# Optimization experiments

Hardware: AMD Instinct MI355X
Metric: run time of the kernel (lower is better)

## Reference

```python
import jax, jax.numpy as jnp
import numpy as np

B, PS, D, HEADS, HD, PROP = 16, 32, 768, 8, 24, 4
N = PS * PS          # 1024 tokens
M = PROP * PROP      # 16 proposal centers
INNER = HEADS * HD   # 192
HID = 4 * D          # 3072
EPS = 1e-12


def setup_inputs() -> dict:
    key = jax.random.key(0)
    ks = jax.random.split(key, 8)
    s = 0.02
    f32 = jnp.float32
    return {
        "x": jax.random.normal(ks[0], (B, N, D), f32),
        "ln1_w": jnp.ones((D,), f32), "ln1_b": jnp.zeros((D,), f32),
        "f_w": jax.random.normal(ks[1], (INNER, D), f32) * s, "f_b": jnp.zeros((INNER,), f32),
        "v_w": jax.random.normal(ks[2], (INNER, D), f32) * s, "v_b": jnp.zeros((INNER,), f32),
        "proj_w": jax.random.normal(ks[3], (D, INNER), f32) * s, "proj_b": jnp.zeros((D,), f32),
        "sim_alpha": jnp.ones((1,), f32), "sim_beta": jnp.zeros((1,), f32),
        "ln2_w": jnp.ones((D,), f32), "ln2_b": jnp.zeros((D,), f32),
        "fc1_w": jax.random.normal(ks[4], (HID, D), f32) * s, "fc1_b": jnp.zeros((HID,), f32),
        "fc2_w": jax.random.normal(ks[5], (D, HID), f32) * s, "fc2_b": jnp.zeros((D,), f32),
    }


def _ln(x, w, b):
    mu = x.mean(-1, keepdims=True)
    var = ((x - mu) ** 2).mean(-1, keepdims=True)
    return (x - mu) / jnp.sqrt(var + 1e-5) * w + b


def _cluster2d(x, f_w, f_b, v_w, v_b, proj_w, proj_b, alpha, beta):
    b = x.shape[0]
    xi = x.reshape(b, PS, PS, D).transpose(0, 3, 1, 2)  # b c w h
    # 1x1 convs f and v
    f = jnp.einsum('oc,bcwh->bowh', f_w, xi) + f_b[None, :, None, None]
    v = jnp.einsum('oc,bcwh->bowh', v_w, xi) + v_b[None, :, None, None]
    # split heads: (b e) c w h
    f = f.reshape(b * HEADS, HD, PS, PS)
    v = v.reshape(b * HEADS, HD, PS, PS)
    # adaptive avg pool to (PROP, PROP) -- exact kernel/stride pooling since PS % PROP == 0
    s = PS // PROP
    cen = f.reshape(-1, HD, PROP, s, PROP, s).mean((3, 5))  # be c 4 4
    vcen = v.reshape(-1, HD, PROP, s, PROP, s).mean((3, 5)).reshape(-1, HD, M).transpose(0, 2, 1)  # be M c
    cf = cen.reshape(-1, HD, M).transpose(0, 2, 1)  # be M c
    xf = f.reshape(-1, HD, N).transpose(0, 2, 1)    # be N c
    # pairwise euclidean similarity on L2-normalized vectors: ||a-b|| = sqrt(2 - 2 a.b)
    cn = cf / jnp.maximum(jnp.linalg.norm(cf, axis=-1, keepdims=True), EPS)
    xn = xf / jnp.maximum(jnp.linalg.norm(xf, axis=-1, keepdims=True), EPS)
    dist = jnp.sqrt(jnp.clip(2.0 - 2.0 * jnp.einsum('bmc,bnc->bmn', cn, xn), EPS, None))
    sim = jax.nn.leaky_relu(beta + alpha * jnp.exp(-dist), 0.2)  # be M N (dropout eval = identity)
    # top-1 hard assignment (torch scatter of argmax -> one-hot mask, no grad through mask)
    mask = jax.nn.one_hot(jnp.argmax(sim, axis=1), M, dtype=sim.dtype).transpose(0, 2, 1)  # be M N
    sim = sim * mask
    v2 = v.reshape(-1, HD, N).transpose(0, 2, 1)  # be N c
    # weighted reduce to centers, then broadcast back to tokens
    outc = (jnp.einsum('bmn,bnc->bmc', sim, v2) + vcen) / (mask.sum(-1, keepdims=True) + 1.0)  # be M c
    out = jnp.einsum('bmn,bmc->bnc', sim, outc)  # be N c
    out = out.reshape(-1, PS, PS, HD).transpose(0, 3, 1, 2).reshape(b, INNER, PS, PS)
    out = jnp.einsum('oc,bcwh->bowh', proj_w, out) + proj_b[None, :, None, None]
    return out.transpose(0, 2, 3, 1).reshape(b, N, D)


def reference(x, ln1_w, ln1_b, f_w, f_b, v_w, v_b, proj_w, proj_b, sim_alpha, sim_beta,
              ln2_w, ln2_b, fc1_w, fc1_b, fc2_w, fc2_b):
    h = x + _cluster2d(_ln(x, ln1_w, ln1_b), f_w, f_b, v_w, v_b, proj_w, proj_b, sim_alpha, sim_beta)
    y = _ln(h, ln2_w, ln2_b)
    y = jax.nn.gelu(jnp.einsum('bnd,hd->bnh', y, fc1_w) + fc1_b, approximate=False)
    y = jnp.einsum('bnh,dh->bnd', y, fc2_w) + fc2_b
    return h + y
```

## Files before the change

### kernel.cpp

```cpp
#include <hip/hip_runtime.h>
#include <hip/hip_bf16.h>
#include <cmath>

typedef unsigned short u16;
typedef short short8 __attribute__((ext_vector_type(8)));
typedef float f32x4 __attribute__((ext_vector_type(4)));

#define D_ 768
#define NTOK 16384
#define INNER_ 192
#define HID_ 3072

__device__ __forceinline__ float u2f(u16 u) { return __uint_as_float((unsigned)u << 16); }
__device__ __forceinline__ u16 f2u(float f) {
  __hip_bfloat16 h = __float2bfloat16(f);
  u16 u; __builtin_memcpy(&u, &h, 2); return u;
}
__device__ __forceinline__ float ld1(const void* p, size_t i, int f32) {
  return f32 ? ((const float*)p)[i] : u2f(((const u16*)p)[i]);
}
__device__ __forceinline__ void st1(void* p, size_t i, float v, int f32) {
  if (f32) ((float*)p)[i] = v; else ((u16*)p)[i] = f2u(v);
}
__device__ __forceinline__ float gelu_exact(float v) {
  return 0.5f * v * (1.f + erff(v * 0.7071067811865476f));
}
__device__ __forceinline__ void unpack8(const uint4 v, float* o) {
  o[0] = u2f((u16)(v.x & 0xffffu)); o[1] = u2f((u16)(v.x >> 16));
  o[2] = u2f((u16)(v.y & 0xffffu)); o[3] = u2f((u16)(v.y >> 16));
  o[4] = u2f((u16)(v.z & 0xffffu)); o[5] = u2f((u16)(v.z >> 16));
  o[6] = u2f((u16)(v.w & 0xffffu)); o[7] = u2f((u16)(v.w >> 16));
}

__global__ __launch_bounds__(64) void detect_kernel(const unsigned* __restrict__ x,
                                                    int* __restrict__ flag) {
  int cnt = 0;
  for (int i = threadIdx.x; i < 512; i += 64) {
    const unsigned e0 = (x[i] >> 7) & 0xFFu;
    if (e0 >= 96u && e0 <= 144u) cnt++;
  }
#pragma unroll
  for (int o = 32; o > 0; o >>= 1) cnt += __shfl_down(cnt, o);
  if (threadIdx.x == 0) flag[0] = (cnt < 256) ? 1 : 0;
}

struct CvtJob { const void* src; u16* dst; int n4; };
struct CvtArgs { CvtJob j[10]; };

__global__ __launch_bounds__(256) void cvt_kernel(CvtArgs a, const int* __restrict__ flagp) {
  const int f32 = flagp[0];
  const CvtJob jb = a.j[blockIdx.y];
  const int i = blockIdx.x * 256 + threadIdx.x;
  if (i >= jb.n4) return;
  if (f32) {
    const float4 v = ((const float4*)jb.src)[i];
    const unsigned lo = (unsigned)f2u(v.x) | ((unsigned)f2u(v.y) << 16);
    const unsigned hi = (unsigned)f2u(v.z) | ((unsigned)f2u(v.w) << 16);
    ((uint2*)jb.dst)[i] = make_uint2(lo, hi);
  } else {
    ((uint2*)jb.dst)[i] = ((const uint2*)jb.src)[i];
  }
}

__global__ __launch_bounds__(256) void ln_kernel(const void* __restrict__ x,
                                                 const void* __restrict__ w,
                                                 const void* __restrict__ b,
                                                 u16* __restrict__ y,
                                                 const int* __restrict__ flagp) {
  const int fl = flagp[0];
  const size_t t = blockIdx.x;
  float v[3];
  float s = 0.f, s2 = 0.f;
#pragma unroll
  for (int i = 0; i < 3; i++) {
    v[i] = ld1(x, t * D_ + threadIdx.x + 256 * i, fl);
    s += v[i];
    s2 += v[i] * v[i];
  }
#pragma unroll
  for (int o = 32; o > 0; o >>= 1) {
    s += __shfl_down(s, o);
    s2 += __shfl_down(s2, o);
  }
  __shared__ float ps[4], ps2[4];
  __shared__ float smu, srstd;
  const int wid = threadIdx.x >> 6, lane = threadIdx.x & 63;
  if (lane == 0) { ps[wid] = s; ps2[wid] = s2; }
  __syncthreads();
  if (threadIdx.x == 0) {
    const float a = ps[0] + ps[1] + ps[2] + ps[3];
    const float a2 = ps2[0] + ps2[1] + ps2[2] + ps2[3];
    const float mu = a * (1.f / D_);
    smu = mu;
    srstd = rsqrtf(a2 * (1.f / D_) - mu * mu + 1e-5f);
  }
  __syncthreads();
  const float mu = smu, rstd = srstd;
#pragma unroll
  for (int i = 0; i < 3; i++) {
    const int c = threadIdx.x + 256 * i;
    y[t * D_ + c] = f2u((v[i] - mu) * rstd * ld1(w, c, fl) + ld1(b, c, fl));
  }
}

template <int EPI>
__global__ __launch_bounds__(256) void mfma_gemm(const u16* __restrict__ A, int lda,
                                                 const u16* __restrict__ B, int ldb,
                                                 const u16* __restrict__ bias,
                                                 const void* __restrict__ res,
                                                 void* __restrict__ C, int ldc,
                                                 int K, int row0,
                                                 const int* __restrict__ flagp) {
  const int fl = flagp[0];
  __shared__ __align__(16) u16 Asb[128 * 32];
  __shared__ __align__(16) u16 Bsb[128 * 32];
  const int tid = threadIdx.x;
  const int lane = tid & 63;
  const int wv = tid >> 6;
  const int bm = blockIdx.x * 128;
  const int bn = blockIdx.y * 128;
  const int wm = (wv & 1) * 64;
  const int wn = (wv >> 1) * 64;
  const int c0 = tid, c1 = tid + 256;
  const u16* Ag0 = A + (size_t)(bm + (c0 >> 2)) * lda + (c0 & 3) * 8;
  const u16* Ag1 = A + (size_t)(bm + (c1 >> 2)) * lda + (c1 & 3) * 8;
  const u16* Bg0 = B + (size_t)(bn + (c0 >> 2)) * ldb + (c0 & 3) * 8;
  const u16* Bg1 = B + (size_t)(bn + (c1 >> 2)) * ldb + (c1 & 3) * 8;
  u16* la0 = &Asb[c0 * 8];
  u16* la1 = &Asb[c1 * 8];
  u16* lb0 = &Bsb[c0 * 8];
  u16* lb1 = &Bsb[c1 * 8];

  f32x4 acc[4][4];
#pragma unroll
  for (int i = 0; i < 4; i++)
#pragma unroll
    for (int j = 0; j < 4; j++) acc[i][j] = (f32x4){0.f, 0.f, 0.f, 0.f};

  const int ml = lane & 15;
  const int kq = (lane >> 4) * 8;

  for (int k0 = 0; k0 < K; k0 += 32) {
    __syncthreads();
    __builtin_amdgcn_global_load_lds(
        (const __attribute__((address_space(1))) void*)(Ag0 + k0),
        (__attribute__((address_space(3))) void*)la0, 16, 0, 0);
    __builtin_amdgcn_global_load_lds(
        (const __attribute__((address_space(1))) void*)(Ag1 + k0),
        (__attribute__((address_space(3))) void*)la1, 16, 0, 0);
    __builtin_amdgcn_global_load_lds(
        (const __attribute__((address_space(1))) void*)(Bg0 + k0),
        (__attribute__((address_space(3))) void*)lb0, 16, 0, 0);
    __builtin_amdgcn_global_load_lds(
        (const __attribute__((address_space(1))) void*)(Bg1 + k0),
        (__attribute__((address_space(3))) void*)lb1, 16, 0, 0);
    __syncthreads();
    short8 af[4], bf[4];
#pragma unroll
    for (int i = 0; i < 4; i++) {
      af[i] = *(const short8*)&Asb[(wm + i * 16 + ml) * 32 + kq];
      bf[i] = *(const short8*)&Bsb[(wn + i * 16 + ml) * 32 + kq];
    }
#pragma unroll
    for (int i = 0; i < 4; i++)
#pragma unroll
      for (int j = 0; j < 4; j++)
        acc[i][j] = __builtin_amdgcn_mfma_f32_16x16x32_bf16(af[i], bf[j], acc[i][j], 0, 0, 0);
  }

  const int qr = (lane >> 4) * 4;
#pragma unroll
  for (int i = 0; i < 4; i++) {
#pragma unroll
    for (int j = 0; j < 4; j++) {
      const int colg = bn + wn + j * 16 + ml;
      const float bb = u2f(bias[colg]);
#pragma unroll
      for (int r = 0; r < 4; r++) {
        const size_t row = (size_t)row0 + bm + wm + i * 16 + qr + r;
        float v = acc[i][j][r] + bb;
        if (EPI == 1) v = gelu_exact(v);
        if (EPI == 2) {
          v += ld1(res, row * ldc + colg, fl);
          st1(C, row * ldc + colg, v, fl);
        } else {
          ((u16*)C)[row * ldc + colg] = f2u(v);
        }
      }
    }
  }
}

#define SB8 __builtin_amdgcn_sched_barrier(0)
#define BAR8 __builtin_amdgcn_s_barrier()

template <int EPI>
__global__ __launch_bounds__(512, 4) void mfma_gemmP(const u16* __restrict__ A, int lda,
                                                     const u16* __restrict__ B, int ldb,
                                                     const u16* __restrict__ bias,
                                                     const void* __restrict__ res,
                                                     void* __restrict__ C, int ldc,
                                                     int K, int row0, int gm, int gn,
                                                     const int* __restrict__ flagp) {
  const int fl = flagp[0];
  __shared__ __align__(16) u16 L[3][(128 + 256) * 32];
  const int tid = threadIdx.x;
  const int lane = tid & 63;
  const int wv = tid >> 6;

  int mb_, nb_;
  {
    const int bid = blockIdx.x;
    const int ntot = gm * gn;
    if ((ntot & 511) == 0 && (512 % gm) == 0 && gm >= 2) {
      const int l = bid >> 8, p = bid & 255;
      const int G = gm >> 1;
      nb_ = (l >> 1) * (512 / gm) + p / G;
      mb_ = (p % G) * 2 + (l & 1);
    } else {
      mb_ = bid % gm;
      nb_ = bid / gm;
    }
  }
  const int bm = mb_ * 128;
  const int bn = nb_ * 256;

  const int wm = (wv & 1) * 64;
  const int wn = (wv >> 1) * 64;
  const int ml = lane & 15;
  const int qk = lane >> 4;

  const int srow = tid >> 2;
  const int q_s = (tid & 3) ^ ((srow >> 1) & 3);
  const size_t gaA  = (size_t)(bm + srow) * lda + q_s * 8;
  const size_t gbB0 = (size_t)(bn + srow) * ldb + q_s * 8;
  const size_t gbB1 = (size_t)(bn + srow + 128) * ldb + q_s * 8;

  int offA[4], offB[4];
#pragma unroll
  for (int i = 0; i < 4; i++) {
    const int r = wm + i * 16 + ml;
    offA[i] = (r * 4 + (qk ^ ((r >> 1) & 3))) * 8;
  }
#pragma unroll
  for (int j = 0; j < 4; j++) {
    const int r = wn + j * 16 + ml;
    offB[j] = 4096 + (r * 4 + (qk ^ ((r >> 1) & 3))) * 8;
  }

  f32x4 acc[4][4];
#pragma unroll
  for (int i = 0; i < 4; i++)
#pragma unroll
    for (int j = 0; j < 4; j++) acc[i][j] = (f32x4){0.f, 0.f, 0.f, 0.f};

  const int NT = K >> 5;

#define STGP(tilex) do {                                                            \
    const size_t k_ = (size_t)(tilex) * 32;                                         \
    u16* lb_ = &L[(tilex) % 3][0];                                                  \
    __builtin_amdgcn_global_load_lds(                                               \
        (const __attribute__((address_space(1))) void*)(A + gaA + k_),              \
        (__attribute__((address_space(3))) void*)(lb_ + tid * 8), 16, 0, 0);        \
    __builtin_amdgcn_global_load_lds(                                               \
        (const __attribute__((address_space(1))) void*)(B + gbB0 + k_),             \
        (__attribute__((address_space(3))) void*)(lb_ + 4096 + tid * 8), 16, 0, 0); \
    __builtin_amdgcn_global_load_lds(                                               \
        (const __attribute__((address_space(1))) void*)(B + gbB1 + k_),             \
        (__attribute__((address_space(3))) void*)(lb_ + 4096 + (tid + 512) * 8), 16, 0, 0); \
  } while (0)

  STGP(0);
  if (NT > 1) {
    STGP(1);
    asm volatile("s_waitcnt vmcnt(3)" ::: "memory");
  } else {
    asm volatile("s_waitcnt vmcnt(0)" ::: "memory");
  }
  SB8; BAR8; SB8;

  for (int t = 0; t < NT; t++) {
    const u16* Lb = &L[t % 3][0];
    short8 af[4], bf[4];
#pragma unroll
    for (int j = 0; j < 4; j++) bf[j] = *(const short8*)(Lb + offB[j]);
#pragma unroll
    for (int i = 0; i < 4; i++) af[i] = *(const short8*)(Lb + offA[i]);
    if (t + 2 < NT) {
      STGP(t + 2);
      asm volatile("s_waitcnt vmcnt(3)" ::: "memory");
    } else if (t + 1 < NT) {
      asm volatile("s_waitcnt vmcnt(0)" ::: "memory");
    }
    SB8; BAR8;
    asm volatile("s_waitcnt lgkmcnt(0)" ::: "memory"); SB8;
    __builtin_amdgcn_s_setprio(1);
#pragma unroll
    for (int i = 0; i < 4; i++)
#pragma unroll
      for (int j = 0; j < 4; j++)
        acc[i][j] = __builtin_amdgcn_mfma_f32_16x16x32_bf16(af[i], bf[j], acc[i][j], 0, 0, 0);
    __builtin_amdgcn_s_setprio(0);
    SB8; BAR8;
  }
#undef STGP

  const int qr = (lane >> 4) * 4;
#pragma unroll
  for (int i = 0; i < 4; i++) {
#pragma unroll
    for (int j = 0; j < 4; j++) {
      const int colg = bn + wn + j * 16 + ml;
      const float bb = u2f(bias[colg]);
#pragma unroll
      for (int r = 0; r < 4; r++) {
        const size_t row = (size_t)row0 + bm + wm + i * 16 + qr + r;
        float v = acc[i][j][r] + bb;
        if (EPI == 1) v = gelu_exact(v);
        if (EPI == 2) {
          v += ld1(res, row * ldc + colg, fl);
          st1(C, row * ldc + colg, v, fl);
        } else {
          ((u16*)C)[row * ldc + colg] = f2u(v);
        }
      }
    }
  }
}

__global__ __launch_bounds__(512) void cluster_kernel(u16* __restrict__ FV,
                                                      const void* __restrict__ alpha_p,
                                                      const void* __restrict__ beta_p,
                                                      const int* __restrict__ flagp) {
  const int fl = flagp[0];
  const int be = blockIdx.x;
  const int b = be >> 3, e = be & 7;
  const int tid = threadIdx.x;
  const float alpha = ld1(alpha_p, 0, fl), beta = ld1(beta_p, 0, fl);

  __shared__ __align__(16) u16 S[1024 * 24];
  __shared__ float cn[16][24];
  __shared__ float vcen[16][24];
  __shared__ float outc[16][24];
  __shared__ float rcn[16];
  __shared__ int cnt[16];

  u16* Fg = FV + ((size_t)b * 1024) * 384 + e * 24;
  const u16* Vg = Fg + 192;

  for (int c = tid; c < 3072; c += 512) {
    const int n = c / 3, q = c - n * 3;
    *(uint4*)&S[n * 24 + q * 8] = *(const uint4*)(Fg + (size_t)n * 384 + q * 8);
  }
  if (tid < 16) cnt[tid] = 0;
  __syncthreads();

  for (int t = tid; t < 384; t += 512) {
    const int m = t / 24, ch = t - m * 24;
    const int pw = m >> 2, ph = m & 3;
    float sum = 0.f;
    for (int dw = 0; dw < 8; dw++) {
      const int base = (pw * 8 + dw) * 32 + ph * 8;
      for (int dh = 0; dh < 8; dh++) sum += u2f(S[(base + dh) * 24 + ch]);
    }
    cn[m][ch] = sum * (1.f / 64.f);
  }
  __syncthreads();
  if (tid < 16) {
    float s = 0.f;
    for (int ch = 0; ch < 24; ch++) { const float v = cn[tid][ch]; s += v * v; }
    rcn[tid] = 1.f / fmaxf(sqrtf(s), 1e-12f);
  }
  __syncthreads();

  const int na = tid, nb = tid + 512;
  float besta = -3.4e38f, bestb = -3.4e38f;
  int bma = 0, bmb = 0;
  {
    float xa[24], xb[24];
    const uint4* ra = (const uint4*)&S[na * 24];
    const uint4* rb = (const uint4*)&S[nb * 24];
#pragma unroll
    for (int q = 0; q < 3; q++) {
      unpack8(ra[q], &xa[q * 8]);
      unpack8(rb[q], &xb[q * 8]);
    }
    float ssa = 0.f, ssb = 0.f;
#pragma unroll
    for (int ch = 0; ch < 24; ch++) {
      ssa = fmaf(xa[ch], xa[ch], ssa);
      ssb = fmaf(xb[ch], xb[ch], ssb);
    }
    const float rna = 1.f / fmaxf(sqrtf(ssa), 1e-12f);
    const float rnb = 1.f / fmaxf(sqrtf(ssb), 1e-12f);
    for (int m = 0; m < 16; m++) {
      float da = 0.f, db = 0.f;
#pragma unroll
      for (int k = 0; k < 12; k++) {
        const float2 c = *(const float2*)&cn[m][2 * k];
        da = fmaf(c.x, xa[2 * k], da); da = fmaf(c.y, xa[2 * k + 1], da);
        db = fmaf(c.x, xb[2 * k], db); db = fmaf(c.y, xb[2 * k + 1], db);
      }
      const float rc = rcn[m];
      da *= rna * rc;
      db *= rnb * rc;
      const float dda = sqrtf(fmaxf(2.f - 2.f * da, 1e-12f));
      const float ddb = sqrtf(fmaxf(2.f - 2.f * db, 1e-12f));
      const float za = beta + alpha * expf(-dda);
      const float zb = beta + alpha * expf(-ddb);
      const float sa = (za >= 0.f) ? za : 0.2f * za;
      const float sb = (zb >= 0.f) ? zb : 0.2f * zb;
      if (sa > besta) { besta = sa; bma = m; }
      if (sb > bestb) { bestb = sb; bmb = m; }
    }
    atomicAdd(&cnt[bma], 1);
    atomicAdd(&cnt[bmb], 1);
  }
  __syncthreads();

  for (int c = tid; c < 3072; c += 512) {
    const int n = c / 3, q = c - n * 3;
    *(uint4*)&S[n * 24 + q * 8] = *(const uint4*)(Vg + (size_t)n * 384 + q * 8);
  }
  if (tid < 384) outc[tid / 24][tid - (tid / 24) * 24] = 0.f;
  __syncthreads();

  for (int t = tid; t < 384; t += 512) {
    const int m = t / 24, ch = t - m * 24;
    const int pw = m >> 2, ph = m & 3;
    float sum = 0.f;
    for (int dw = 0; dw < 8; dw++) {
      const int base = (pw * 8 + dw) * 32 + ph * 8;
      for (int dh = 0; dh < 8; dh++) sum += u2f(S[(base + dh) * 24 + ch]);
    }
    vcen[m][ch] = sum * (1.f / 64.f);
  }

  {
    float va[24], vb[24];
    const uint4* ra = (const uint4*)&S[na * 24];
    const uint4* rb = (const uint4*)&S[nb * 24];
#pragma unroll
    for (int q = 0; q < 3; q++) {
      unpack8(ra[q], &va[q * 8]);
      unpack8(rb[q], &vb[q * 8]);
    }
#pragma unroll
    for (int ch = 0; ch < 24; ch++) {
      atomicAdd(&outc[bma][ch], besta * va[ch]);
      atomicAdd(&outc[bmb][ch], bestb * vb[ch]);
    }
  }
  __syncthreads();

  for (int t = tid; t < 384; t += 512) {
    const int m = t / 24, ch = t - m * 24;
    outc[m][ch] = (outc[m][ch] + vcen[m][ch]) / ((float)cnt[m] + 1.f);
  }
  __syncthreads();

#pragma unroll
  for (int pass = 0; pass < 2; pass++) {
    const int n = pass ? nb : na;
    const int m = pass ? bmb : bma;
    const float s = pass ? bestb : besta;
    unsigned w[12];
#pragma unroll
    for (int k = 0; k < 12; k++) {
      w[k] = (unsigned)f2u(s * outc[m][2 * k]) |
             ((unsigned)f2u(s * outc[m][2 * k + 1]) << 16);
    }
    uint4* dst = (uint4*)(Fg + (size_t)n * 384);
    dst[0] = make_uint4(w[0], w[1], w[2], w[3]);
    dst[1] = make_uint4(w[4], w[5], w[6], w[7]);
    dst[2] = make_uint4(w[8], w[9], w[10], w[11]);
  }
}

extern "C" void kernel_launch(void* const* d_in, const int* in_sizes, int n_in,
                              void* d_out, int out_size, void* d_ws, size_t ws_size,
                              hipStream_t stream) {
  const void* x      = d_in[0];
  const void* ln1_w  = d_in[1];
  const void* ln1_b  = d_in[2];
  const void* f_w    = d_in[3];
  const void* f_b    = d_in[4];
  const void* v_w    = d_in[5];
  const void* v_b    = d_in[6];
  const void* proj_w = d_in[7];
  const void* proj_b = d_in[8];
  const void* alpha  = d_in[9];
  const void* beta   = d_in[10];
  const void* ln2_w  = d_in[11];
  const void* ln2_b  = d_in[12];
  const void* fc1_w  = d_in[13];
  const void* fc1_b  = d_in[14];
  const void* fc2_w  = d_in[15];
  const void* fc2_b  = d_in[16];

  char* ws = (char*)d_ws;
  int* flag  = (int*)(ws + 0);
  u16* fvw   = (u16*)(ws + 256);
  u16* prw   = (u16*)(ws + 590080);
  u16* f1w   = (u16*)(ws + 884992);
  u16* f2w   = (u16*)(ws + 5603584);
  u16* fvb   = (u16*)(ws + 10322176);
  u16* prb   = (u16*)(ws + 10322944);
  u16* f1b   = (u16*)(ws + 10324480);
  u16* f2b_  = (u16*)(ws + 10330624);
  u16* Y1    = (u16*)(ws + 10332416);
  u16* FV    = (u16*)(ws + 35498240);
  u16* Gext  = (u16*)(ws + 48081152);

  const long extra = (long)ws_size - 48081152L;
  u16* G; long crows;
  if (extra >= (long)NTOK * HID_ * 2) { G = Gext; crows = NTOK; }
  else if (extra >= 256L * HID_ * 2) { G = Gext; crows = (extra / (HID_ * 2)) / 256 * 256; }
  else { G = FV; crows = 2048; }

  detect_kernel<<<1, 64, 0, stream>>>((const unsigned*)x, flag);

  CvtArgs ca;
  ca.j[0] = {f_w,    fvw,            147456 / 4};
  ca.j[1] = {v_w,    fvw + 147456,   147456 / 4};
  ca.j[2] = {proj_w, prw,            147456 / 4};
  ca.j[3] = {fc1_w,  f1w,            2359296 / 4};
  ca.j[4] = {fc2_w,  f2w,            2359296 / 4};
  ca.j[5] = {f_b,    fvb,            192 / 4};
  ca.j[6] = {v_b,    fvb + 192,      192 / 4};
  ca.j[7] = {proj_b, prb,            768 / 4};
  ca.j[8] = {fc1_b,  f1b,            3072 / 4};
  ca.j[9] = {fc2_b,  f2b_,           768 / 4};
  cvt_kernel<<<dim3(2304, 10), 256, 0, stream>>>(ca, flag);

  ln_kernel<<<NTOK, 256, 0, stream>>>(x, ln1_w, ln1_b, Y1, flag);
  mfma_gemm<0><<<dim3(128, 3), 256, 0, stream>>>(
      Y1, D_, fvw, D_, fvb, nullptr, FV, 384, D_, 0, flag);
  cluster_kernel<<<128, 512, 0, stream>>>(FV, alpha, beta, flag);
  mfma_gemm<2><<<dim3(128, 6), 256, 0, stream>>>(
      FV, 384, prw, INNER_, prb, x, d_out, D_, INNER_, 0, flag);
  ln_kernel<<<NTOK, 256, 0, stream>>>(d_out, ln2_w, ln2_b, Y1, flag);
  for (long t0 = 0; t0 < NTOK; t0 += crows) {
    const long ct = (t0 + crows <= NTOK) ? crows : (NTOK - t0);
    const int gm1 = (int)(ct / 128), gn1 = HID_ / 256;
    const int gm2 = (int)(ct / 128), gn2 = D_ / 256;
    mfma_gemmP<1><<<dim3(gm1 * gn1), 512, 0, stream>>>(
        Y1 + t0 * D_, D_, f1w, D_, f1b, nullptr, G, HID_, D_, 0, gm1, gn1, flag);
    mfma_gemmP<2><<<dim3(gm2 * gn2), 512, 0, stream>>>(
        G, HID_, f2w, HID_, f2b_, d_out, d_out, D_, HID_, (int)t0, gm2, gn2, flag);
  }
}
```

Baseline: 488.1 us.

## Retile MLP GEMMs to 256x128 blocks and restructure cluster kernel

Replaces the 512-thread 128x256 MLP GEMM, which used a swizzled block order, with a 256-thread 256x128 tile kernel. Each wave now holds an 8x4 MFMA accumulator grid, which raises per-wave register pressure and drops the block remapping meant for L2 locality. The cluster kernel now runs 1024 threads, one token each, and loads F and V into separate LDS buffers so the two centroid pools are computed in one pass. It writes results to a new CL buffer instead of overwriting FV, which changes the projection GEMM's A stride and shifts the workspace layout.

New measurement: 530.7 us. +8.7%, slower.

```diff
diff --git a/kernel.cpp b/kernel.cpp
--- a/kernel.cpp
+++ b/kernel.cpp
@@ -195,85 +195,82 @@
 #define BAR8 __builtin_amdgcn_s_barrier()
 
 template <int EPI>
-__global__ __launch_bounds__(512, 4) void mfma_gemmP(const u16* __restrict__ A, int lda,
+__global__ __launch_bounds__(256, 2) void mfma_gemmQ(const u16* __restrict__ A, int lda,
                                                      const u16* __restrict__ B, int ldb,
                                                      const u16* __restrict__ bias,
                                                      const void* __restrict__ res,
                                                      void* __restrict__ C, int ldc,
-                                                     int K, int row0, int gm, int gn,
+                                                     int K, int row0,
                                                      const int* __restrict__ flagp) {
   const int fl = flagp[0];
-  __shared__ __align__(16) u16 L[3][(128 + 256) * 32];
+  __shared__ __align__(16) u16 L[3][(256 + 128) * 32];
   const int tid = threadIdx.x;
   const int lane = tid & 63;
   const int wv = tid >> 6;
 
-  int mb_, nb_;
-  {
-    const int bid = blockIdx.x;
-    const int ntot = gm * gn;
-    if ((ntot & 511) == 0 && (512 % gm) == 0 && gm >= 2) {
-      const int l = bid >> 8, p = bid & 255;
-      const int G = gm >> 1;
-      nb_ = (l >> 1) * (512 / gm) + p / G;
-      mb_ = (p % G) * 2 + (l & 1);
-    } else {
-      mb_ = bid % gm;
-      nb_ = bid / gm;
-    }
-  }
-  const int bm = mb_ * 128;
-  const int bn = nb_ * 256;
-
-  const int wm = (wv & 1) * 64;
+  const int bm = blockIdx.x * 256;
+  const int bn = blockIdx.y * 128;
+
+  const int wm = (wv & 1) * 128;
   const int wn = (wv >> 1) * 64;
   const int ml = lane & 15;
   const int qk = lane >> 4;
 
   const int srow = tid >> 2;
   const int q_s = (tid & 3) ^ ((srow >> 1) & 3);
-  const size_t gaA  = (size_t)(bm + srow) * lda + q_s * 8;
-  const size_t gbB0 = (size_t)(bn + srow) * ldb + q_s * 8;
-  const size_t gbB1 = (size_t)(bn + srow + 128) * ldb + q_s * 8;
-
-  int offA[4], offB[4];
-#pragma unroll
-  for (int i = 0; i < 4; i++) {
+  size_t gA[4], gB[2];
+#pragma unroll
+  for (int p = 0; p < 4; p++) gA[p] = (size_t)(bm + srow + 64 * p) * lda + q_s * 8;
+#pragma unroll
+  for (int p = 0; p < 2; p++) gB[p] = (size_t)(bn + srow + 64 * p) * ldb + q_s * 8;
+
+  int offA[8], offB[4];
+#pragma unroll
+  for (int i = 0; i < 8; i++) {
     const int r = wm + i * 16 + ml;
     offA[i] = (r * 4 + (qk ^ ((r >> 1) & 3))) * 8;
   }
 #pragma unroll
   for (int j = 0; j < 4; j++) {
     const int r = wn + j * 16 + ml;
-    offB[j] = 4096 + (r * 4 + (qk ^ ((r >> 1) & 3))) * 8;
-  }
-
-  f32x4 acc[4][4];
-#pragma unroll
-  for (int i = 0; i < 4; i++)
+    offB[j] = 8192 + (r * 4 + (qk ^ ((r >> 1) & 3))) * 8;
+  }
+
+  f32x4 acc[8][4];
+#pragma unroll
+  for (int i = 0; i < 8; i++)
 #pragma unroll
     for (int j = 0; j < 4; j++) acc[i][j] = (f32x4){0.f, 0.f, 0.f, 0.f};
 
   const int NT = K >> 5;
 
-#define STGP(tilex) do {                                                            \
+#define STGQ(tilex) do {                                                            \
     const size_t k_ = (size_t)(tilex) * 32;                                         \
     u16* lb_ = &L[(tilex) % 3][0];                                                  \
     __builtin_amdgcn_global_load_lds(                                               \
-        (const __attribute__((address_space(1))) void*)(A + gaA + k_),              \
+        (const __attribute__((address_space(1))) void*)(A + gA[0] + k_),            \
         (__attribute__((address_space(3))) void*)(lb_ + tid * 8), 16, 0, 0);        \
     __builtin_amdgcn_global_load_lds(                                               \
-        (const __attribute__((address_space(1))) void*)(B + gbB0 + k_),             \
-        (__attribute__((address_space(3))) void*)(lb_ + 4096 + tid * 8), 16, 0, 0); \
+        (const __attribute__((address_space(1))) void*)(A + gA[1] + k_),            \
+        (__attribute__((address_space(3))) void*)(lb_ + (tid + 256) * 8), 16, 0, 0);\
     __builtin_amdgcn_global_load_lds(                                               \
-        (const __attribute__((address_space(1))) void*)(B + gbB1 + k_),             \
-        (__attribute__((address_space(3))) void*)(lb_ + 4096 + (tid + 512) * 8), 16, 0, 0); \
+        (const __attribute__((address_space(1))) void*)(A + gA[2] + k_),            \
+        (__attribute__((address_space(3))) void*)(lb_ + (tid + 512) * 8), 16, 0, 0);\
+    __builtin_amdgcn_global_load_lds(                                               \
+        (const __attribute__((address_space(1))) void*)(A + gA[3] + k_),            \
+        (__attribute__((address_space(3))) void*)(lb_ + (tid + 768) * 8), 16, 0, 0);\
+    __builtin_amdgcn_global_load_lds(                                               \
+        (const __attribute__((address_space(1))) void*)(B + gB[0] + k_),            \
+        (__attribute__((address_space(3))) void*)(lb_ + 8192 + tid * 8), 16, 0, 0); \
+    __builtin_amdgcn_global_load_lds(                                               \
+        (const __attribute__((address_space(1))) void*)(B + gB[1] + k_),            \
+        (__attribute__((address_space(3))) void*)(lb_ + 8192 + (tid + 256) * 8), 16, 0, 0); \
   } while (0)
 
-  STGP(0);
+  STGQ(0);
   if (NT > 1) {
-    STGP(1);
-    asm volatile("s_waitcnt vmcnt(3)" ::: "memory");
+    STGQ(1);
+    asm volatile("s_waitcnt vmcnt(6)" ::: "memory");
   } else {
     asm volatile("s_waitcnt vmcnt(0)" ::: "memory");
   }
@@ -281,14 +278,14 @@
 
   for (int t = 0; t < NT; t++) {
     const u16* Lb = &L[t % 3][0];
-    short8 af[4], bf[4];
+    short8 af[8], bf[4];
 #pragma unroll
     for (int j = 0; j < 4; j++) bf[j] = *(const short8*)(Lb + offB[j]);
 #pragma unroll
-    for (int i = 0; i < 4; i++) af[i] = *(const short8*)(Lb + offA[i]);
+    for (int i = 0; i < 8; i++) af[i] = *(const short8*)(Lb + offA[i]);
     if (t + 2 < NT) {
-      STGP(t + 2);
-      asm volatile("s_waitcnt vmcnt(3)" ::: "memory");
+      STGQ(t + 2);
+      asm volatile("s_waitcnt vmcnt(6)" ::: "memory");
     } else if (t + 1 < NT) {
       asm volatile("s_waitcnt vmcnt(0)" ::: "memory");
     }
@@ -296,18 +293,18 @@
     asm volatile("s_waitcnt lgkmcnt(0)" ::: "memory"); SB8;
     __builtin_amdgcn_s_setprio(1);
 #pragma unroll
-    for (int i = 0; i < 4; i++)
+    for (int i = 0; i < 8; i++)
 #pragma unroll
       for (int j = 0; j < 4; j++)
         acc[i][j] = __builtin_amdgcn_mfma_f32_16x16x32_bf16(af[i], bf[j], acc[i][j], 0, 0, 0);
     __builtin_amdgcn_s_setprio(0);
     SB8; BAR8;
   }
-#undef STGP
+#undef STGQ
 
   const int qr = (lane >> 4) * 4;
 #pragma unroll
-  for (int i = 0; i < 4; i++) {
+  for (int i = 0; i < 8; i++) {
 #pragma unroll
     for (int j = 0; j < 4; j++) {
       const int colg = bn + wn + j * 16 + ml;
@@ -328,42 +325,50 @@
   }
 }
 
-__global__ __launch_bounds__(512) void cluster_kernel(u16* __restrict__ FV,
-                                                      const void* __restrict__ alpha_p,
-                                                      const void* __restrict__ beta_p,
-                                                      const int* __restrict__ flagp) {
+__global__ __launch_bounds__(1024) void cluster_kernel(const u16* __restrict__ FV,
+                                                       u16* __restrict__ CL,
+                                                       const void* __restrict__ alpha_p,
+                                                       const void* __restrict__ beta_p,
+                                                       const int* __restrict__ flagp) {
   const int fl = flagp[0];
   const int be = blockIdx.x;
   const int b = be >> 3, e = be & 7;
   const int tid = threadIdx.x;
   const float alpha = ld1(alpha_p, 0, fl), beta = ld1(beta_p, 0, fl);
 
-  __shared__ __align__(16) u16 S[1024 * 24];
+  __shared__ __align__(16) u16 SF[1024 * 24];
+  __shared__ __align__(16) u16 SV[1024 * 24];
   __shared__ float cn[16][24];
   __shared__ float vcen[16][24];
   __shared__ float outc[16][24];
   __shared__ float rcn[16];
   __shared__ int cnt[16];
 
-  u16* Fg = FV + ((size_t)b * 1024) * 384 + e * 24;
+  const u16* Fg = FV + ((size_t)b * 1024) * 384 + e * 24;
   const u16* Vg = Fg + 192;
-
-  for (int c = tid; c < 3072; c += 512) {
+  u16* Cg = CL + ((size_t)b * 1024) * 192 + e * 24;
+
+  for (int c = tid; c < 3072; c += 1024) {
     const int n = c / 3, q = c - n * 3;
-    *(uint4*)&S[n * 24 + q * 8] = *(const uint4*)(Fg + (size_t)n * 384 + q * 8);
+    *(uint4*)&SF[n * 24 + q * 8] = *(const uint4*)(Fg + (size_t)n * 384 + q * 8);
+    *(uint4*)&SV[n * 24 + q * 8] = *(const uint4*)(Vg + (size_t)n * 384 + q * 8);
   }
   if (tid < 16) cnt[tid] = 0;
-  __syncthreads();
-
-  for (int t = tid; t < 384; t += 512) {
+  if (tid < 384) outc[tid / 24][tid - (tid / 24) * 24] = 0.f;
+  __syncthreads();
+
+  if (tid < 768) {
+    const int t = tid & 383;
     const int m = t / 24, ch = t - m * 24;
     const int pw = m >> 2, ph = m & 3;
+    const u16* src = (tid < 384) ? SF : SV;
     float sum = 0.f;
     for (int dw = 0; dw < 8; dw++) {
       const int base = (pw * 8 + dw) * 32 + ph * 8;
-      for (int dh = 0; dh < 8; dh++) sum += u2f(S[(base + dh) * 24 + ch]);
-    }
-    cn[m][ch] = sum * (1.f / 64.f);
+      for (int dh = 0; dh < 8; dh++) sum += u2f(src[(base + dh) * 24 + ch]);
+    }
+    if (tid < 384) cn[m][ch] = sum * (1.f / 64.f);
+    else           vcen[m][ch] = sum * (1.f / 64.f);
   }
   __syncthreads();
   if (tid < 16) {
@@ -373,104 +378,55 @@
   }
   __syncthreads();
 
-  const int na = tid, nb = tid + 512;
-  float besta = -3.4e38f, bestb = -3.4e38f;
-  int bma = 0, bmb = 0;
+  const int n = tid;
+  float best = -3.4e38f;
+  int bm_ = 0;
   {
-    float xa[24], xb[24];
-    const uint4* ra = (const uint4*)&S[na * 24];
-    const uint4* rb = (const uint4*)&S[nb * 24];
-#pragma unroll
-    for (int q = 0; q < 3; q++) {
-      unpack8(ra[q], &xa[q * 8]);
-      unpack8(rb[q], &xb[q * 8]);
-    }
-    float ssa = 0.f, ssb = 0.f;
-#pragma unroll
-    for (int ch = 0; ch < 24; ch++) {
-      ssa = fmaf(xa[ch], xa[ch], ssa);
-      ssb = fmaf(xb[ch], xb[ch], ssb);
-    }
-    const float rna = 1.f / fmaxf(sqrtf(ssa), 1e-12f);
-    const float rnb = 1.f / fmaxf(sqrtf(ssb), 1e-12f);
+    float xf[24];
+    const uint4* ra = (const uint4*)&SF[n * 24];
+#pragma unroll
+    for (int q = 0; q < 3; q++) unpack8(ra[q], &xf[q * 8]);
+    float ss = 0.f;
+#pragma unroll
+    for (int ch = 0; ch < 24; ch++) ss = fmaf(xf[ch], xf[ch], ss);
+    const float rn = 1.f / fmaxf(sqrtf(ss), 1e-12f);
     for (int m = 0; m < 16; m++) {
-      float da = 0.f, db = 0.f;
+      float d = 0.f;
 #pragma unroll
       for (int k = 0; k < 12; k++) {
         const float2 c = *(const float2*)&cn[m][2 * k];
-        da = fmaf(c.x, xa[2 * k], da); da = fmaf(c.y, xa[2 * k + 1], da);
-        db = fmaf(c.x, xb[2 * k], db); db = fmaf(c.y, xb[2 * k + 1], db);
+        d = fmaf(c.x, xf[2 * k], d); d = fmaf(c.y, xf[2 * k + 1], d);
       }
-      const float rc = rcn[m];
-      da *= rna * rc;
-      db *= rnb * rc;
-      const float dda = sqrtf(fmaxf(2.f - 2.f * da, 1e-12f));
-      const float ddb = sqrtf(fmaxf(2.f - 2.f * db, 1e-12f));
-      const float za = beta + alpha * expf(-dda);
-      const float zb = beta + alpha * expf(-ddb);
-      const float sa = (za >= 0.f) ? za : 0.2f * za;
-      const float sb = (zb >= 0.f) ? zb : 0.2f * zb;
-      if (sa > besta) { besta = sa; bma = m; }
-      if (sb > bestb) { bestb = sb; bmb = m; }
-    }
-    atomicAdd(&cnt[bma], 1);
-    atomicAdd(&cnt[bmb], 1);
-  }
-  __syncthreads();
-
-  for (int c = tid; c < 3072; c += 512) {
-    const int n = c / 3, q = c - n * 3;
-    *(uint4*)&S[n * 24 + q * 8] = *(const uint4*)(Vg + (size_t)n * 384 + q * 8);
-  }
-  if (tid < 384) outc[tid / 24][tid - (tid / 24) * 24] = 0.f;
-  __syncthreads();
-
-  for (int t = tid; t < 384; t += 512) {
-    const int m = t / 24, ch = t - m * 24;
-    const int pw = m >> 2, ph = m & 3;
-    float sum = 0.f;
-    for (int dw = 0; dw < 8; dw++) {
-      const int base = (pw * 8 + dw) * 32 + ph * 8;
-      for (int dh = 0; dh < 8; dh++) sum += u2f(S[(base + dh) * 24 + ch]);
-    }
-    vcen[m][ch] = sum * (1.f / 64.f);
-  }
+      d *= rn * rcn[m];
+      const float dd = sqrtf(fmaxf(2.f - 2.f * d, 1e-12f));
+      const float z = beta + alpha * expf(-dd);
+      const float sim = (z >= 0.f) ? z : 0.2f * z;
+      if (sim > best) { best = sim; bm_ = m; }
+    }
+    atomicAdd(&cnt[bm_], 1);
+    float vf[24];
+    const uint4* rv = (const uint4*)&SV[n * 24];
+#pragma unroll
+    for (int q = 0; q < 3; q++) unpack8(rv[q], &vf[q * 8]);
+#pragma unroll
+    for (int ch = 0; ch < 24; ch++) atomicAdd(&outc[bm_][ch], best * vf[ch]);
+  }
+  __syncthreads();
+
+  if (tid < 384) {
+    const int m = tid / 24, ch = tid - m * 24;
+    outc[m][ch] = (outc[m][ch] + vcen[m][ch]) / ((float)cnt[m] + 1.f);
+  }
+  __syncthreads();
 
   {
-    float va[24], vb[24];
-    const uint4* ra = (const uint4*)&S[na * 24];
-    const uint4* rb = (const uint4*)&S[nb * 24];
-#pragma unroll
-    for (int q = 0; q < 3; q++) {
-      unpack8(ra[q], &va[q * 8]);
-      unpack8(rb[q], &vb[q * 8]);
-    }
-#pragma unroll
-    for (int ch = 0; ch < 24; ch++) {
-      atomicAdd(&outc[bma][ch], besta * va[ch]);
-      atomicAdd(&outc[bmb][ch], bestb * vb[ch]);
-    }
-  }
-  __syncthreads();
-
-  for (int t = tid; t < 384; t += 512) {
-    const int m = t / 24, ch = t - m * 24;
-    outc[m][ch] = (outc[m][ch] + vcen[m][ch]) / ((float)cnt[m] + 1.f);
-  }
-  __syncthreads();
-
-#pragma unroll
-  for (int pass = 0; pass < 2; pass++) {
-    const int n = pass ? nb : na;
-    const int m = pass ? bmb : bma;
-    const float s = pass ? bestb : besta;
     unsigned w[12];
 #pragma unroll
     for (int k = 0; k < 12; k++) {
-      w[k] = (unsigned)f2u(s * outc[m][2 * k]) |
-             ((unsigned)f2u(s * outc[m][2 * k + 1]) << 16);
-    }
-    uint4* dst = (uint4*)(Fg + (size_t)n * 384);
+      w[k] = (unsigned)f2u(best * outc[bm_][2 * k]) |
+             ((unsigned)f2u(best * outc[bm_][2 * k + 1]) << 16);
+    }
+    uint4* dst = (uint4*)(Cg + (size_t)n * 192);
     dst[0] = make_uint4(w[0], w[1], w[2], w[3]);
     dst[1] = make_uint4(w[4], w[5], w[6], w[7]);
     dst[2] = make_uint4(w[8], w[9], w[10], w[11]);
@@ -510,9 +466,10 @@
   u16* f2b_  = (u16*)(ws + 10330624);
   u16* Y1    = (u16*)(ws + 10332416);
   u16* FV    = (u16*)(ws + 35498240);
-  u16* Gext  = (u16*)(ws + 48081152);
-
-  const long extra = (long)ws_size - 48081152L;
+  u16* CL    = (u16*)(ws + 48081152);
+  u16* Gext  = (u16*)(ws + 54372608);
+
+  const long extra = (long)ws_size - 54372608L;
   u16* G; long crows;
   if (extra >= (long)NTOK * HID_ * 2) { G = Gext; crows = NTOK; }
   else if (extra >= 256L * HID_ * 2) { G = Gext; crows = (extra / (HID_ * 2)) / 256 * 256; }
@@ -536,17 +493,15 @@
   ln_kernel<<<NTOK, 256, 0, stream>>>(x, ln1_w, ln1_b, Y1, flag);
   mfma_gemm<0><<<dim3(128, 3), 256, 0, stream>>>(
       Y1, D_, fvw, D_, fvb, nullptr, FV, 384, D_, 0, flag);
-  cluster_kernel<<<128, 512, 0, stream>>>(FV, alpha, beta, flag);
+  cluster_kernel<<<128, 1024, 0, stream>>>(FV, CL, alpha, beta, flag);
   mfma_gemm<2><<<dim3(128, 6), 256, 0, stream>>>(
-      FV, 384, prw, INNER_, prb, x, d_out, D_, INNER_, 0, flag);
+      CL, INNER_, prw, INNER_, prb, x, d_out, D_, INNER_, 0, flag);
   ln_kernel<<<NTOK, 256, 0, stream>>>(d_out, ln2_w, ln2_b, Y1, flag);
   for (long t0 = 0; t0 < NTOK; t0 += crows) {
     const long ct = (t0 + crows <= NTOK) ? crows : (NTOK - t0);
-    const int gm1 = (int)(ct / 128), gn1 = HID_ / 256;
-    const int gm2 = (int)(ct / 128), gn2 = D_ / 256;
-    mfma_gemmP<1><<<dim3(gm1 * gn1), 512, 0, stream>>>(
-        Y1 + t0 * D_, D_, f1w, D_, f1b, nullptr, G, HID_, D_, 0, gm1, gn1, flag);
-    mfma_gemmP<2><<<dim3(gm2 * gn2), 512, 0, stream>>>(
-        G, HID_, f2w, HID_, f2b_, d_out, d_out, D_, HID_, (int)t0, gm2, gn2, flag);
-  }
-}
+    mfma_gemmQ<1><<<dim3(ct / 256, HID_ / 128), 256, 0, stream>>>(
+        Y1 + t0 * D_, D_, f1w, D_, f1b, nullptr, G, HID_, D_, 0, flag);
+    mfma_gemmQ<2><<<dim3(ct / 256, D_ / 128), 256, 0, stream>>>(
+        G, HID_, f2w, HID_, f2b_, d_out, d_out, D_, HID_, (int)t0, flag);
+  }
+}
```
